# Kernel tuning notes

Measured on AMD Instinct MI355X. Metric: run time of the kernel, lower is better.

The kernel has to match this reference:

```python
import jax, jax.numpy as jnp
from jax import lax
import numpy as np

B, H, W = 8, 96, 96
CIN, COUT, QD, NH = 256, 128, 32, 8
LA_MID = COUT // 8  # 16
GRIDS = (6, 3, 2, 1)
EPS = 1e-5  # torch BatchNorm default eps


def conv2d(x, w):
    # 'same' padding for 3x3 stride 1 (autopad k//2)
    return lax.conv_general_dilated(x, w, (1, 1), 'SAME',
                                    dimension_numbers=('NCHW', 'OIHW', 'NCHW'))


def bn2d(x, g, b, m, v):
    inv = g / jnp.sqrt(v + EPS)
    return x * inv[None, :, None, None] + (b - m * inv)[None, :, None, None]


def adaptive_avg_pool_tokens(x, oh, ow):
    # matches torch adaptive_avg_pool2d bin edges; returns [b, c, oh*ow]
    b, c, h, w = x.shape
    cells = []
    for i in range(oh):
        h0, h1 = (i * h) // oh, -((-(i + 1) * h) // oh)
        for j in range(ow):
            w0, w1 = (j * w) // ow, -((-(j + 1) * w) // ow)
            cells.append(x[:, :, h0:h1, w0:w1].mean(axis=(2, 3)))
    return jnp.stack(cells, axis=-1)


def psp(x, grids):
    b, c, h, w = x.shape
    ar = w / h
    return jnp.concatenate(
        [adaptive_avg_pool_tokens(x, g, max(1, round(ar * g))) for g in grids], axis=2)


def setup_inputs() -> dict:
    key = jax.random.key(0)
    ks = jax.random.split(key, 9)
    f = jnp.float32
    return {
        'x': jax.random.normal(ks[0], (B, CIN, H, W), f),
        'w_red': jax.random.normal(ks[1], (COUT, CIN, 3, 3), f) * 0.02,
        'bng': jnp.ones((COUT,), f), 'bnb': jnp.zeros((COUT,), f),
        'bnm': jnp.zeros((COUT,), f), 'bnv': jnp.ones((COUT,), f),
        'w_q': jax.random.normal(ks[2], (QD, COUT), f) * 0.1,
        'b_q': jnp.zeros((QD,), f),
        'w_k': jax.random.normal(ks[3], (QD, COUT), f) * 0.1,
        'b_k': jnp.zeros((QD,), f),
        'w_v': jax.random.normal(ks[4], (COUT, COUT), f) * 0.08,
        'b_v': jnp.zeros((COUT,), f),
        'lsh': jax.random.normal(ks[5], (NH, QD), f),
        'w_la1': jax.random.normal(ks[6], (LA_MID, COUT), f) * 0.1,
        'lag': jnp.ones((LA_MID,), f), 'lab': jnp.zeros((LA_MID,), f),
        'lam': jnp.zeros((LA_MID,), f), 'lav': jnp.ones((LA_MID,), f),
        'w_la2': jax.random.normal(ks[7], (COUT, LA_MID, 3, 3), f) * 0.02,
    }


def reference(x, w_red, bng, bnb, bnm, bnv, w_q, b_q, w_k, b_k, w_v, b_v,
              lsh, w_la1, lag, lab, lam, lav, w_la2):
    # reduce_channel: Conv(256,128,3) = conv + BN + SiLU
    xr = jax.nn.silu(bn2d(conv2d(x, w_red), bng, bnb, bnm, bnv))  # [B,COUT,H,W]
    b, c, h, w = xr.shape
    # query: 1x1 conv to 32 ch, flatten spatial -> [B, HW, QD]
    q = (jnp.einsum('oc,bchw->bohw', w_q, xr)
         + b_q[None, :, None, None]).reshape(b, QD, h * w).transpose(0, 2, 1)
    # key_psp and value_psp act on the same xr -> identical token sets [B,COUT,50]
    tokens = psp(xr, GRIDS)
    k_tok = (jnp.einsum('oc,bcn->bon', w_k, tokens)
             + b_k[None, :, None]).transpose(0, 2, 1)  # [B,50,QD]
    v_tok = (jnp.einsum('oc,bcn->bon', w_v, tokens)
             + b_v[None, :, None]).transpose(0, 2, 1)  # [B,50,COUT]
    # ReformerAttention: argmax over TOKEN dim -> [B, NH]; sort indices lie in [0,NH)
    # so the gather picks a per-batch permutation of the first NH key/value tokens
    # (faithful to the torch code; q_buckets is computed but unused there).
    k_buckets = jnp.argmax(jnp.einsum('hd,bnd->bhn', lsh, k_tok), axis=-1)  # [B,NH]
    k_idx = jnp.argsort(k_buckets, axis=-1)  # [B,NH], values in [0,NH)
    k_s = jnp.take_along_axis(k_tok, k_idx[:, :, None], axis=1)  # [B,NH,QD]
    v_s = jnp.take_along_axis(v_tok, k_idx[:, :, None], axis=1)  # [B,NH,COUT]
    att = jax.nn.softmax(jnp.einsum('bqd,bkd->bqk', q, k_s), axis=-1)  # [B,HW,NH]
    ctx = jnp.einsum('bqk,bkd->bqd', att, v_s).transpose(0, 2, 1).reshape(b, COUT, h, w)
    # LocalAttenModule: Conv(128,16,1)(conv+bn+silu) -> 3x3 conv 16->128 -> tanh mask
    y = jax.nn.silu(bn2d(jnp.einsum('oc,bchw->bohw', w_la1, ctx), lag, lab, lam, lav))
    mask = jnp.tanh(conv2d(y, w_la2))
    ctx = ctx * mask + ctx
    return xr + ctx
```

## Files before the change

kernel.cpp:

```cpp
#include <hip/hip_runtime.h>
#include <hip/hip_bf16.h>
#include <cmath>

typedef __attribute__((ext_vector_type(8))) short short8;
typedef __attribute__((ext_vector_type(4))) short s16x4;
typedef __attribute__((ext_vector_type(4))) float f32x4;
typedef unsigned short u16;

#define HW 9216

__device__ inline float bf2f(u16 u) {
    union { unsigned int i; float f; } x; x.i = ((unsigned int)u) << 16; return x.f;
}
__device__ inline u16 f2bf(float f) {
    union { unsigned int i; float f; } x; x.f = f;
    unsigned int r = x.i + 0x7FFF + ((x.i >> 16) & 1);
    return (u16)(r >> 16);
}

__global__ __launch_bounds__(256) void transform_w(
    const float* __restrict__ wred, const float* __restrict__ wla2,
    u16* __restrict__ Wt1, u16* __restrict__ Wt2)
{
    int idx = blockIdx.x * 256 + threadIdx.x;
    if (idx < 128 * 2304) {
        int co = idx / 2304;
        int rem = idx - co * 2304;
        int c = rem / 288;
        int r2 = rem - c * 288;
        int khw = r2 >> 5, ciL = r2 & 31;
        Wt1[idx] = f2bf(wred[((co * 256 + c * 32 + ciL) * 9 + khw)]);
    } else {
        int i2 = idx - 128 * 2304;
        if (i2 < 128 * 160) {
            int co = i2 / 160;
            int k = i2 - co * 160;
            int khw = k >> 4, ci = k & 15;
            Wt2[i2] = (khw < 9) ? f2bf(wla2[((co << 4) + ci) * 9 + khw]) : (u16)0;
        }
    }
}

__global__ __launch_bounds__(256) void transpose_x(
    const float* __restrict__ X, u16* __restrict__ Xt)
{
    int bid = blockIdx.x;
    int b = bid & 7, chunk = bid >> 3;
    int p = chunk * 256 + threadIdx.x;
    const float* xb = X + (size_t)b * 256 * HW + p;
    u16* ot = Xt + ((size_t)b * HW + p) * 256;
    for (int oct = 0; oct < 32; ++oct) {
        short8 v;
#pragma unroll
        for (int j = 0; j < 8; ++j)
            v[j] = (short)f2bf(xb[(size_t)(oct * 8 + j) * HW]);
        *(short8*)(ot + oct * 8) = v;
    }
}

template<int CIN, int KTILES, int KP, int EPI>
__global__ __launch_bounds__(256) void conv_k(
    const u16* __restrict__ Xt, const u16* __restrict__ Wt,
    u16* OutH, float* OutF,
    const float* __restrict__ bg, const float* __restrict__ bb,
    const float* __restrict__ bm, const float* __restrict__ bv,
    const u16* __restrict__ xrb, const float* ctxf)
{
    const int LDB = 40;
    __shared__ __align__(16) short As[2][128 * 40];
    __shared__ __align__(16) short Bs[2][96 * 40];
    __shared__ float invA[128], betA[128];

    const int tid = threadIdx.x;
    const int bid = blockIdx.x;
    const int b = bid & 7;
    const int tile = bid >> 3;
    const int w0 = (tile % 3) * 32;
    const int h0 = (tile / 3) * 3;

    const int lane = tid & 63;
    const int wid = tid >> 6;
    const int wm = (wid & 1) * 64;
    const int wn = (wid >> 1) * 48;
    const int r = lane & 15;
    const int quad = lane >> 4;

    if constexpr (EPI == 1) {
        if (tid < 128) {
            float iv = bg[tid] * rsqrtf(bv[tid] + 1e-5f);
            invA[tid] = iv;
            betA[tid] = bb[tid] - bm[tid] * iv;
        }
    }

    const int p = tid & 127;
    const int o_lo = tid >> 7;

    const u16* XtB = Xt + (size_t)b * HW * CIN;
    const short8 z8 = {0, 0, 0, 0, 0, 0, 0, 0};

    short8 aR0, aR1, bR0, bR1;

    auto loadB = [&](int slot, int kt) -> short8 {
        int row = slot >> 2, o = slot & 3;
        int pw = row & 31, ph = row >> 5;
        int hgl = h0 + ph, wgl = w0 + pw;
        if (CIN == 256) {
            int c = (kt * 57) >> 9;
            int khw = kt - c * 9;
            int dh = (khw * 11) >> 5;
            int dw = khw - 3 * dh;
            int hh = hgl + dh - 1, ww = wgl + dw - 1;
            bool ok = ((unsigned)hh < 96u) && ((unsigned)ww < 96u);
            const u16* src = XtB + ((size_t)hh * 96 + ww) * 256 + c * 32 + o * 8;
            return ok ? *(const short8*)src : z8;
        } else {
            int kg = kt * 32 + o * 8;
            int khw = kg >> 4, ci0 = kg & 15;
            int dh = (khw * 11) >> 5, dw = khw - 3 * dh;
            int hh = hgl + dh - 1, ww = wgl + dw - 1;
            bool ok = ((unsigned)hh < 96u) && ((unsigned)ww < 96u) && (khw < 9);
            const u16* src = XtB + ((size_t)hh * 96 + ww) * 16 + ci0;
            return ok ? *(const short8*)src : z8;
        }
    };

    auto stage = [&](int kt) {
        aR0 = *(const short8*)(Wt + (size_t)p * KP + kt * 32 + o_lo * 8);
        aR1 = *(const short8*)(Wt + (size_t)p * KP + kt * 32 + (o_lo + 2) * 8);
        bR0 = loadB(tid, kt);
        if (tid < 128) bR1 = loadB(256 + tid, kt);
    };
    auto commit = [&](int buf) {
        *(short8*)(&As[buf][p * LDB + o_lo * 8]) = aR0;
        *(short8*)(&As[buf][p * LDB + (o_lo + 2) * 8]) = aR1;
        *(short8*)(&Bs[buf][(tid >> 2) * LDB + (tid & 3) * 8]) = bR0;
        if (tid < 128) {
            int s = 256 + tid;
            *(short8*)(&Bs[buf][(s >> 2) * LDB + (s & 3) * 8]) = bR1;
        }
    };

    f32x4 acc[4][3];
    f32x4 zz = {0.f, 0.f, 0.f, 0.f};
#pragma unroll
    for (int i = 0; i < 4; i++)
#pragma unroll
        for (int j = 0; j < 3; j++) acc[i][j] = zz;

    stage(0);
    commit(0);
    __syncthreads();

    for (int kt = 0; kt < KTILES; ++kt) {
        int cur = kt & 1;
        if (kt + 1 < KTILES) stage(kt + 1);
        short8 af[4], bfr[3];
#pragma unroll
        for (int i = 0; i < 4; i++)
            af[i] = *(const short8*)(&As[cur][(wm + i * 16 + r) * LDB + quad * 8]);
#pragma unroll
        for (int j = 0; j < 3; j++)
            bfr[j] = *(const short8*)(&Bs[cur][(wn + j * 16 + r) * LDB + quad * 8]);
#pragma unroll
        for (int i = 0; i < 4; i++)
#pragma unroll
            for (int j = 0; j < 3; j++)
                acc[i][j] = __builtin_amdgcn_mfma_f32_16x16x32_bf16(af[i], bfr[j], acc[i][j], 0, 0, 0);
        if (kt + 1 < KTILES) {
            commit(cur ^ 1);
            __syncthreads();
        }
    }

#pragma unroll
    for (int i = 0; i < 4; i++) {
#pragma unroll
        for (int j = 0; j < 3; j++) {
            int pl = wn + j * 16 + r;
            int w = w0 + (pl & 31), h = h0 + (pl >> 5);
#pragma unroll
            for (int g = 0; g < 4; ++g) {
                int co = wm + i * 16 + quad * 4 + g;
                float v = acc[i][j][g];
                size_t oidx = ((size_t)b * 128 + co) * HW + h * 96 + w;
                if constexpr (EPI == 1) {
                    float val = v * invA[co] + betA[co];
                    float sv = val / (1.f + __expf(-val));
                    OutH[oidx] = f2bf(sv);
                } else {
                    float xv = bf2f(xrb[oidx]);
                    float cv = ctxf[oidx];
                    float e = __expf(2.f * v);
                    float th = 1.f - 2.f / (e + 1.f);
                    OutF[oidx] = xv + cv * (1.f + th);
                }
            }
        }
    }
}

__global__ __launch_bounds__(256) void prep_attn(
    const u16* __restrict__ xr,
    const float* __restrict__ wk, const float* __restrict__ bk,
    const float* __restrict__ wv, const float* __restrict__ bv,
    const float* __restrict__ wq, const float* __restrict__ bq,
    float* __restrict__ Aout, float* __restrict__ Vout, float* __restrict__ c0out)
{
    __shared__ float part[256];
    __shared__ float tok[128];
    __shared__ float ks[32];
    int t = threadIdx.x;
    int bid = blockIdx.x;
    int b = bid & 7, n = bid >> 3;
    int c = t & 127, half = t >> 7;
    int i0 = (n < 6) ? 0 : 16;
    int j0 = ((n < 6) ? n : (n - 6)) * 16;
    const u16* xb = xr + (size_t)(b * 128 + c) * HW;

    float s = 0.f;
    for (int rr = 0; rr < 8; ++rr) {
        int row = i0 + half * 8 + rr;
        const u16* rp = xb + row * 96 + j0;
        short8 v0 = *(const short8*)rp;
        short8 v1 = *(const short8*)(rp + 8);
#pragma unroll
        for (int j = 0; j < 8; ++j) s += bf2f((u16)v0[j]) + bf2f((u16)v1[j]);
    }
    part[t] = s;
    __syncthreads();
    if (t < 128) tok[t] = (part[t] + part[t + 128]) * (1.f / 256.f);
    __syncthreads();
    if (t < 32) {
        float s2 = bk[t];
        for (int cc = 0; cc < 128; ++cc) s2 += wk[t * 128 + cc] * tok[cc];
        ks[t] = s2;
    }
    __syncthreads();
    if (t < 128) {
        float s3 = bv[c];
        for (int c2 = 0; c2 < 128; ++c2) s3 += wv[c * 128 + c2] * tok[c2];
        Vout[((size_t)b * 8 + n) * 128 + c] = s3;
    } else {
        float s4 = 0.f;
        for (int d = 0; d < 32; ++d) s4 += wq[d * 128 + c] * ks[d];
        Aout[((size_t)b * 8 + n) * 128 + c] = s4;
    }
    if (t == 0) {
        float s5 = 0.f;
        for (int d = 0; d < 32; ++d) s5 += bq[d] * ks[d];
        c0out[b * 8 + n] = s5;
    }
}

__global__ __launch_bounds__(256) void attn_k(
    const u16* __restrict__ xr,
    const float* __restrict__ Ain, const float* __restrict__ Vin,
    const float* __restrict__ c0in,
    const float* __restrict__ wla1,
    const float* __restrict__ lag, const float* __restrict__ lab,
    const float* __restrict__ lam, const float* __restrict__ lav,
    float* __restrict__ ctxout, u16* __restrict__ yout)
{
    __shared__ float Xs[128 * 64];
    __shared__ float As[8 * 128], Vs[8 * 128], Ws[16 * 128];
    __shared__ float satt[8 * 64];
    __shared__ float c0s[8], inv1[16], bet1[16];

    int t = threadIdx.x;
    int bid = blockIdx.x;
    int b = bid & 7;
    int p0 = (bid >> 3) * 64;

    for (int i = t; i < 1024; i += 256) { As[i] = Ain[b * 1024 + i]; Vs[i] = Vin[b * 1024 + i]; }
    for (int i = t; i < 2048; i += 256) Ws[i] = wla1[i];
    if (t < 8) c0s[t] = c0in[b * 8 + t];
    if (t < 16) {
        float iv = lag[t] * rsqrtf(lav[t] + 1e-5f);
        inv1[t] = iv; bet1[t] = lab[t] - lam[t] * iv;
    }
    const u16* xb = xr + (size_t)b * 128 * HW + p0;
#pragma unroll
    for (int it = 0; it < 4; ++it) {
        int c = (t >> 3) + it * 32;
        int seg = t & 7;
        short8 v = *(const short8*)(xb + (size_t)c * HW + seg * 8);
#pragma unroll
        for (int j = 0; j < 8; ++j) Xs[c * 64 + seg * 8 + j] = bf2f((u16)v[j]);
    }
    __syncthreads();
    {
        int pp = t & 63, ng = t >> 6;
        float a0 = 0.f, a1 = 0.f;
        for (int c = 0; c < 128; ++c) {
            float x = Xs[c * 64 + pp];
            a0 += As[(ng * 2) * 128 + c] * x;
            a1 += As[(ng * 2 + 1) * 128 + c] * x;
        }
        satt[(ng * 2) * 64 + pp] = a0 + c0s[ng * 2];
        satt[(ng * 2 + 1) * 64 + pp] = a1 + c0s[ng * 2 + 1];
    }
    __syncthreads();
    if (t < 64) {
        float m = -1e30f;
        float sv[8];
#pragma unroll
        for (int n = 0; n < 8; ++n) { sv[n] = satt[n * 64 + t]; m = fmaxf(m, sv[n]); }
        float sum = 0.f;
#pragma unroll
        for (int n = 0; n < 8; ++n) { sv[n] = __expf(sv[n] - m); sum += sv[n]; }
        float rcp = 1.f / sum;
#pragma unroll
        for (int n = 0; n < 8; ++n) satt[n * 64 + t] = sv[n] * rcp;
    }
    __syncthreads();
    {
        int pp = t & 63, cg = t >> 6;
        float at[8];
#pragma unroll
        for (int n = 0; n < 8; ++n) at[n] = satt[n * 64 + pp];
        for (int ci = 0; ci < 32; ++ci) {
            int c = cg * 32 + ci;
            float s = 0.f;
#pragma unroll
            for (int n = 0; n < 8; ++n) s += at[n] * Vs[n * 128 + c];
            ctxout[((size_t)b * 128 + c) * HW + p0 + pp] = s;
            Xs[c * 64 + pp] = s;
        }
    }
    __syncthreads();
    {
        int pp = t & 63, dg = t >> 6;
        float a[4] = {0.f, 0.f, 0.f, 0.f};
        for (int c = 0; c < 128; ++c) {
            float x = Xs[c * 64 + pp];
#pragma unroll
            for (int k = 0; k < 4; ++k) a[k] += Ws[(dg * 4 + k) * 128 + c] * x;
        }
        s16x4 pk;
#pragma unroll
        for (int k = 0; k < 4; ++k) {
            int d = dg * 4 + k;
            float val = a[k] * inv1[d] + bet1[d];
            float s = val / (1.f + __expf(-val));
            pk[k] = (short)f2bf(s);
        }
        *(s16x4*)(yout + ((size_t)b * HW + p0 + pp) * 16 + dg * 4) = pk;
    }
}

extern "C" void kernel_launch(void* const* d_in, const int* in_sizes, int n_in,
                              void* d_out, int out_size, void* d_ws, size_t ws_size,
                              hipStream_t stream)
{
    const float* x    = (const float*)d_in[0];
    const float* wred = (const float*)d_in[1];
    const float* bng  = (const float*)d_in[2];
    const float* bnb  = (const float*)d_in[3];
    const float* bnm  = (const float*)d_in[4];
    const float* bnv  = (const float*)d_in[5];
    const float* wq   = (const float*)d_in[6];
    const float* bq   = (const float*)d_in[7];
    const float* wk   = (const float*)d_in[8];
    const float* bk   = (const float*)d_in[9];
    const float* wv   = (const float*)d_in[10];
    const float* bv   = (const float*)d_in[11];
    const float* wla1 = (const float*)d_in[13];
    const float* lag  = (const float*)d_in[14];
    const float* lab  = (const float*)d_in[15];
    const float* lam  = (const float*)d_in[16];
    const float* lav  = (const float*)d_in[17];
    const float* wla2 = (const float*)d_in[18];

    char* ws = (char*)d_ws;
    u16*   xr  = (u16*)(ws + 0);
    u16*   yt  = (u16*)(ws + 18874368);
    u16*   Wt1 = (u16*)(ws + 21233664);
    u16*   Wt2 = (u16*)(ws + 21823488);
    float* Ab  = (float*)(ws + 21864448);
    float* Vb  = (float*)(ws + 21897216);
    float* c0b = (float*)(ws + 21929984);
    u16*   xt   = (u16*)d_out;
    float* outp = (float*)d_out;

    transform_w<<<dim3(1232), dim3(256), 0, stream>>>(wred, wla2, Wt1, Wt2);

    transpose_x<<<dim3(288), dim3(256), 0, stream>>>(x, xt);

    conv_k<256, 72, 2304, 1><<<dim3(768), dim3(256), 0, stream>>>(
        xt, Wt1, xr, nullptr, bng, bnb, bnm, bnv, nullptr, nullptr);

    prep_attn<<<dim3(64), dim3(256), 0, stream>>>(xr, wk, bk, wv, bv, wq, bq, Ab, Vb, c0b);

    attn_k<<<dim3(1152), dim3(256), 0, stream>>>(
        xr, Ab, Vb, c0b, wla1, lag, lab, lam, lav, outp, yt);

    conv_k<16, 5, 160, 2><<<dim3(768), dim3(256), 0, stream>>>(
        yt, Wt2, nullptr, outp, nullptr, nullptr, nullptr, nullptr, xr, outp);
}
```

Before: 324.7 us.

## Load conv tiles directly into LDS via global_load_lds and raise MFMA priority

Measured after the change: 309.4 us. -4.7%, faster.

```diff
diff --git a/kernel.cpp b/kernel.cpp
--- a/kernel.cpp
+++ b/kernel.cpp
@@ -16,6 +16,13 @@
     union { unsigned int i; float f; } x; x.f = f;
     unsigned int r = x.i + 0x7FFF + ((x.i >> 16) & 1);
     return (u16)(r >> 16);
+}
+
+__device__ inline void gload16(const u16* g, u16* l) {
+    __builtin_amdgcn_global_load_lds(
+        (const __attribute__((address_space(1))) void*)g,
+        (__attribute__((address_space(3))) void*)l,
+        16, 0, 0);
 }
 
 __global__ __launch_bounds__(256) void transform_w(
@@ -64,11 +71,11 @@
     u16* OutH, float* OutF,
     const float* __restrict__ bg, const float* __restrict__ bb,
     const float* __restrict__ bm, const float* __restrict__ bv,
-    const u16* __restrict__ xrb, const float* ctxf)
-{
-    const int LDB = 40;
-    __shared__ __align__(16) short As[2][128 * 40];
-    __shared__ __align__(16) short Bs[2][96 * 40];
+    const u16* __restrict__ xrb, const float* ctxf,
+    const u16* __restrict__ zp)
+{
+    __shared__ __align__(16) short As[2][128 * 32];
+    __shared__ __align__(16) short Bs[2][96 * 32];
     __shared__ float invA[128], betA[128];
 
     const int tid = threadIdx.x;
@@ -93,15 +100,9 @@
         }
     }
 
-    const int p = tid & 127;
-    const int o_lo = tid >> 7;
-
     const u16* XtB = Xt + (size_t)b * HW * CIN;
-    const short8 z8 = {0, 0, 0, 0, 0, 0, 0, 0};
-
-    short8 aR0, aR1, bR0, bR1;
-
-    auto loadB = [&](int slot, int kt) -> short8 {
+
+    auto bsrc = [&](int slot, int kt) -> const u16* {
         int row = slot >> 2, o = slot & 3;
         int pw = row & 31, ph = row >> 5;
         int hgl = h0 + ph, wgl = w0 + pw;
@@ -112,33 +113,26 @@
             int dw = khw - 3 * dh;
             int hh = hgl + dh - 1, ww = wgl + dw - 1;
             bool ok = ((unsigned)hh < 96u) && ((unsigned)ww < 96u);
-            const u16* src = XtB + ((size_t)hh * 96 + ww) * 256 + c * 32 + o * 8;
-            return ok ? *(const short8*)src : z8;
+            return ok ? XtB + ((size_t)hh * 96 + ww) * 256 + c * 32 + o * 8 : zp;
         } else {
             int kg = kt * 32 + o * 8;
             int khw = kg >> 4, ci0 = kg & 15;
             int dh = (khw * 11) >> 5, dw = khw - 3 * dh;
             int hh = hgl + dh - 1, ww = wgl + dw - 1;
             bool ok = ((unsigned)hh < 96u) && ((unsigned)ww < 96u) && (khw < 9);
-            const u16* src = XtB + ((size_t)hh * 96 + ww) * 16 + ci0;
-            return ok ? *(const short8*)src : z8;
+            return ok ? XtB + ((size_t)hh * 96 + ww) * 16 + ci0 : zp;
         }
     };
 
-    auto stage = [&](int kt) {
-        aR0 = *(const short8*)(Wt + (size_t)p * KP + kt * 32 + o_lo * 8);
-        aR1 = *(const short8*)(Wt + (size_t)p * KP + kt * 32 + (o_lo + 2) * 8);
-        bR0 = loadB(tid, kt);
-        if (tid < 128) bR1 = loadB(256 + tid, kt);
-    };
-    auto commit = [&](int buf) {
-        *(short8*)(&As[buf][p * LDB + o_lo * 8]) = aR0;
-        *(short8*)(&As[buf][p * LDB + (o_lo + 2) * 8]) = aR1;
-        *(short8*)(&Bs[buf][(tid >> 2) * LDB + (tid & 3) * 8]) = bR0;
-        if (tid < 128) {
-            int s = 256 + tid;
-            *(short8*)(&Bs[buf][(s >> 2) * LDB + (s & 3) * 8]) = bR1;
-        }
+    auto stage = [&](int kt, int buf) {
+        int sA0 = tid, sA1 = tid + 256;
+        gload16(Wt + (size_t)(sA0 >> 2) * KP + kt * 32 + (sA0 & 3) * 8,
+                (u16*)&As[buf][(64 * wid) * 8]);
+        gload16(Wt + (size_t)(sA1 >> 2) * KP + kt * 32 + (sA1 & 3) * 8,
+                (u16*)&As[buf][(256 + 64 * wid) * 8]);
+        gload16(bsrc(tid, kt), (u16*)&Bs[buf][(64 * wid) * 8]);
+        if (wid < 2)
+            gload16(bsrc(tid + 256, kt), (u16*)&Bs[buf][(256 + 64 * wid) * 8]);
     };
 
     f32x4 acc[4][3];
@@ -148,29 +142,28 @@
 #pragma unroll
         for (int j = 0; j < 3; j++) acc[i][j] = zz;
 
-    stage(0);
-    commit(0);
+    stage(0, 0);
     __syncthreads();
 
     for (int kt = 0; kt < KTILES; ++kt) {
         int cur = kt & 1;
-        if (kt + 1 < KTILES) stage(kt + 1);
+        if (kt + 1 < KTILES) stage(kt + 1, cur ^ 1);
         short8 af[4], bfr[3];
 #pragma unroll
         for (int i = 0; i < 4; i++)
-            af[i] = *(const short8*)(&As[cur][(wm + i * 16 + r) * LDB + quad * 8]);
+            af[i] = *(const short8*)(&As[cur][(wm + i * 16 + r) * 32 + quad * 8]);
 #pragma unroll
         for (int j = 0; j < 3; j++)
-            bfr[j] = *(const short8*)(&Bs[cur][(wn + j * 16 + r) * LDB + quad * 8]);
+            bfr[j] = *(const short8*)(&Bs[cur][(wn + j * 16 + r) * 32 + quad * 8]);
+        __builtin_amdgcn_s_setprio(1);
 #pragma unroll
         for (int i = 0; i < 4; i++)
 #pragma unroll
             for (int j = 0; j < 3; j++)
                 acc[i][j] = __builtin_amdgcn_mfma_f32_16x16x32_bf16(af[i], bfr[j], acc[i][j], 0, 0, 0);
-        if (kt + 1 < KTILES) {
-            commit(cur ^ 1);
+        __builtin_amdgcn_s_setprio(0);
+        if (kt + 1 < KTILES)
             __syncthreads();
-        }
     }
 
 #pragma unroll
@@ -382,13 +375,14 @@
     float* c0b = (float*)(ws + 21929984);
     u16*   xt   = (u16*)d_out;
     float* outp = (float*)d_out;
+    const u16* zp = Wt2 + 144;
 
     transform_w<<<dim3(1232), dim3(256), 0, stream>>>(wred, wla2, Wt1, Wt2);
 
     transpose_x<<<dim3(288), dim3(256), 0, stream>>>(x, xt);
 
     conv_k<256, 72, 2304, 1><<<dim3(768), dim3(256), 0, stream>>>(
-        xt, Wt1, xr, nullptr, bng, bnb, bnm, bnv, nullptr, nullptr);
+        xt, Wt1, xr, nullptr, bng, bnb, bnm, bnv, nullptr, nullptr, zp);
 
     prep_attn<<<dim3(64), dim3(256), 0, stream>>>(xr, wk, bk, wv, bv, wq, bq, Ab, Vb, c0b);
 
@@ -396,5 +390,5 @@
         xr, Ab, Vb, c0b, wla1, lag, lab, lam, lav, outp, yt);
 
     conv_k<16, 5, 160, 2><<<dim3(768), dim3(256), 0, stream>>>(
-        yt, Wt2, nullptr, outp, nullptr, nullptr, nullptr, nullptr, xr, outp);
-}
+        yt, Wt2, nullptr, outp, nullptr, nullptr, nullptr, nullptr, xr, outp, zp);
+}
```
